# Kernel optimization log

Hardware: AMD Instinct MI355X
Metric: run time of the kernel (lower is better)

## Reference

```python
import jax, jax.numpy as jnp
import numpy as np

D_C = 16  # c // 4 with c = 64
BN_EPS = 1e-5


def _block(x, w, b, g, beta, m, v, a):
    """Conv2Dblock with 1x1 conv: pointwise conv -> BatchNorm2d (inference) -> PReLU."""
    y = jnp.einsum('oi,bift->boft', w, x) + b[None, :, None, None]
    scale = (g / jnp.sqrt(v + BN_EPS))[None, :, None, None]
    y = (y - m[None, :, None, None]) * scale + beta[None, :, None, None]
    return jnp.where(y >= 0, y, a * y)  # PReLU, single shared slope


def _asa(inp, fqkv, tqk, proj):
    b, c, f, t = inp.shape
    scale = 1.0 / np.sqrt(D_C)
    neg = -jnp.finfo(inp.dtype).max

    # frequency attention
    f_qkv = _block(inp, *fqkv)                      # [b, 3*d_c interleaved, f, t]
    f_qkv = f_qkv.reshape(b, D_C, 3, f, t)          # '(c k)' split, k fastest
    qf, kf, v = f_qkv[:, :, 0], f_qkv[:, :, 1], f_qkv[:, :, 2]
    f_score = jnp.einsum('bcft,bcyt->btfy', qf, kf) * scale
    f_score = jax.nn.softmax(f_score, axis=-1)
    f_out = jnp.einsum('btfy,bcyt->bcft', f_score, v)

    # causal time attention
    t_qk = _block(inp, *tqk)                        # [b, 2*d_c interleaved, f, t]
    t_qk = t_qk.reshape(b, D_C, 2, f, t)
    qt, kt = t_qk[:, :, 0], t_qk[:, :, 1]
    t_score = jnp.einsum('bcft,bcfy->bfty', qt, kt) * scale
    causal_mask = jnp.triu(jnp.ones((t, t), dtype=bool), 1)  # strictly upper => future
    t_score = jnp.where(causal_mask[None, None], neg, t_score)
    t_score = jax.nn.softmax(t_score, axis=-1)
    t_out = jnp.einsum('bfty,bcfy->bcft', t_score, f_out)

    out = _block(t_out, *proj)
    return out + inp


def setup_inputs() -> dict:
    key = jax.random.key(0)
    ks = jax.random.split(key, 24)
    B, C, F, T = 2, 64, 257, 500
    dc = D_C

    def conv_params(ki, kb, out_ch, in_ch):
        w = jax.random.normal(ki, (out_ch, in_ch), jnp.float32) * (1.0 / np.sqrt(in_ch))
        b = jax.random.normal(kb, (out_ch,), jnp.float32) * 0.02
        return w, b

    inp = jax.random.normal(ks[0], (B, C, F, T), jnp.float32)

    fqkv_w, fqkv_b = conv_params(ks[1], ks[2], 3 * dc, C)
    fqkv_g = 1.0 + 0.1 * jax.random.uniform(ks[3], (3 * dc,), jnp.float32)
    fqkv_beta = 0.02 * jax.random.normal(ks[4], (3 * dc,), jnp.float32)
    fqkv_m = 0.02 * jax.random.normal(ks[5], (3 * dc,), jnp.float32)
    fqkv_v = 0.9 + 0.2 * jax.random.uniform(ks[6], (3 * dc,), jnp.float32)
    fqkv_a = jnp.full((1,), 0.25, jnp.float32)

    tqk_w, tqk_b = conv_params(ks[7], ks[8], 2 * dc, C)
    tqk_g = 1.0 + 0.1 * jax.random.uniform(ks[9], (2 * dc,), jnp.float32)
    tqk_beta = 0.02 * jax.random.normal(ks[10], (2 * dc,), jnp.float32)
    tqk_m = 0.02 * jax.random.normal(ks[11], (2 * dc,), jnp.float32)
    tqk_v = 0.9 + 0.2 * jax.random.uniform(ks[12], (2 * dc,), jnp.float32)
    tqk_a = jnp.full((1,), 0.25, jnp.float32)

    proj_w, proj_b = conv_params(ks[13], ks[14], C, dc)
    proj_g = 1.0 + 0.1 * jax.random.uniform(ks[15], (C,), jnp.float32)
    proj_beta = 0.02 * jax.random.normal(ks[16], (C,), jnp.float32)
    proj_m = 0.02 * jax.random.normal(ks[17], (C,), jnp.float32)
    proj_v = 0.9 + 0.2 * jax.random.uniform(ks[18], (C,), jnp.float32)
    proj_a = jnp.full((1,), 0.25, jnp.float32)

    return dict(inp=inp,
                fqkv_w=fqkv_w, fqkv_b=fqkv_b, fqkv_g=fqkv_g, fqkv_beta=fqkv_beta,
                fqkv_m=fqkv_m, fqkv_v=fqkv_v, fqkv_a=fqkv_a,
                tqk_w=tqk_w, tqk_b=tqk_b, tqk_g=tqk_g, tqk_beta=tqk_beta,
                tqk_m=tqk_m, tqk_v=tqk_v, tqk_a=tqk_a,
                proj_w=proj_w, proj_b=proj_b, proj_g=proj_g, proj_beta=proj_beta,
                proj_m=proj_m, proj_v=proj_v, proj_a=proj_a)


def reference(inp, fqkv_w, fqkv_b, fqkv_g, fqkv_beta, fqkv_m, fqkv_v, fqkv_a,
              tqk_w, tqk_b, tqk_g, tqk_beta, tqk_m, tqk_v, tqk_a,
              proj_w, proj_b, proj_g, proj_beta, proj_m, proj_v, proj_a):
    return _asa(inp,
                (fqkv_w, fqkv_b, fqkv_g, fqkv_beta, fqkv_m, fqkv_v, fqkv_a),
                (tqk_w, tqk_b, tqk_g, tqk_beta, tqk_m, tqk_v, tqk_a),
                (proj_w, proj_b, proj_g, proj_beta, proj_m, proj_v, proj_a))
```

## Files before the change

### kernel.cpp

```cpp
#include <hip/hip_runtime.h>

#define BB 2
#define CIN 64
#define FD 257
#define TD 500
#define FT (FD*TD)
#define EPS 1e-5f
#define NEGINF (-3.0e38f)
#define FDP 260
#define FQT_PLANE (TD*FDP)
#define LOG2E 1.44269504088896f
#define EXP2F(x) __builtin_amdgcn_exp2f(x)

typedef _Float16 half_t;
typedef half_t half2_t __attribute__((ext_vector_type(2)));
typedef half_t half4 __attribute__((ext_vector_type(4)));
typedef float  f32x4 __attribute__((ext_vector_type(4)));

__global__ __launch_bounds__(256) void stage1_kernel(
    const float* __restrict__ x,
    const float* __restrict__ fw, const float* __restrict__ fb_,
    const float* __restrict__ fg, const float* __restrict__ fbe,
    const float* __restrict__ fm, const float* __restrict__ fv_,
    const float* __restrict__ fa,
    const float* __restrict__ tw, const float* __restrict__ tb_,
    const float* __restrict__ tg, const float* __restrict__ tbe,
    const float* __restrict__ tm, const float* __restrict__ tv_,
    const float* __restrict__ ta,
    half_t* __restrict__ fq, half_t* __restrict__ tq)
{
    __shared__ half_t Wh[80][68];
    __shared__ float  Bl[80];
    __shared__ half_t Ob[4][32][80];
    const int tid = threadIdx.x;
    for (int idx = tid; idx < 80*64; idx += 256) {
        const int o = idx >> 6, i = idx & 63;
        float sc, wv;
        if (o < 48) { sc = fg[o]*rsqrtf(fv_[o]+EPS); wv = fw[o*64+i]; }
        else { const int o2 = o-48; sc = tg[o2]*rsqrtf(tv_[o2]+EPS); wv = tw[o2*64+i]; }
        Wh[o][i] = (half_t)(wv*sc);
    }
    if (tid < 80) {
        const int o = tid;
        if (o < 48) Bl[o] = (fb_[o]-fm[o])*(fg[o]*rsqrtf(fv_[o]+EPS)) + fbe[o];
        else { const int o2 = o-48; Bl[o] = (tb_[o2]-tm[o2])*(tg[o2]*rsqrtf(tv_[o2]+EPS)) + tbe[o2]; }
    }
    __syncthreads();
    const float af = fa[0], at = ta[0];
    const int w = tid >> 6, lane = tid & 63;
    const int lmod = lane & 15, ldiv = lane >> 4;
    const int b  = blockIdx.x / 1004;
    const int nb = blockIdx.x % 1004;
    const long n0 = (long)nb*128;

    half4 a[5][4];
    #pragma unroll
    for (int ot = 0; ot < 5; ++ot)
        #pragma unroll
        for (int ks = 0; ks < 4; ++ks)
            a[ot][ks] = *(const half4*)&Wh[16*ot + lmod][16*ks + 4*ldiv];
    f32x4 bias[5];
    #pragma unroll
    for (int ot = 0; ot < 5; ++ot)
        #pragma unroll
        for (int r = 0; r < 4; ++r)
            bias[ot][r] = Bl[16*ot + 4*ldiv + r];

    const float* xplane = x + (long)b*CIN*FT;
    half4 bfr[2][4];
    #pragma unroll
    for (int pt = 0; pt < 2; ++pt) {
        const long p = n0 + 32*w + 16*pt + lmod;
        const long pc = (p < FT) ? p : (FT-1);
        const float* xp = xplane + pc;
        #pragma unroll
        for (int ks = 0; ks < 4; ++ks) {
            #pragma unroll
            for (int e = 0; e < 4; ++e) {
                const int ch = 16*ks + 4*ldiv + e;
                bfr[pt][ks][e] = (half_t)xp[(long)ch*FT];
            }
        }
    }
    #pragma unroll
    for (int pt = 0; pt < 2; ++pt) {
        const int pl = 16*pt + lmod;
        const int msk = ((pl >> 2) & 3) << 2;
        #pragma unroll
        for (int ot = 0; ot < 5; ++ot) {
            f32x4 acc = bias[ot];
            #pragma unroll
            for (int ks = 0; ks < 4; ++ks)
                acc = __builtin_amdgcn_mfma_f32_16x16x16f16(a[ot][ks], bfr[pt][ks], acc, 0, 0, 0);
            const float alpha = (ot < 3) ? af : at;
            half4 hv;
            #pragma unroll
            for (int r = 0; r < 4; ++r) {
                float v = acc[r];
                v = v >= 0.f ? v : alpha*v;
                hv[r] = (half_t)v;
            }
            *(half4*)&Ob[w][pl][(16*ot + 4*ldiv) ^ msk] = hv;
        }
    }
    const int pr = lane & 7, og0 = lane >> 3;
    const long pbase = n0 + 32*w + 4*pr;
    if (pbase < FT) {
        const int msk = (pr & 3) << 2;
        #pragma unroll
        for (int i = 0; i < 10; ++i) {
            const int o = og0 + 8*i;
            half4 hv;
            #pragma unroll
            for (int e = 0; e < 4; ++e) hv[e] = Ob[w][4*pr + e][o ^ msk];
            half_t* dst = (o < 48) ? (fq + ((long)b*48 + o)*FT + pbase)
                                   : (tq + ((long)b*32 + (o-48))*FT + pbase);
            *(half4*)dst = hv;
        }
    }
}

__global__ __launch_bounds__(256) void transpose_h2h_kernel(
    const half_t* __restrict__ src, half_t* __restrict__ dst,
    int R, int C, int CS, int RP)
{
    __shared__ half_t tile[64][68];
    const int plane = blockIdx.x;
    const int rb = blockIdx.y*64, cb = blockIdx.z*64;
    const half_t* s = src + (long)plane*R*CS;
    half_t* d = dst + (long)plane*C*RP;
    const int q4 = (threadIdx.x & 15)*4;
    const int wl = threadIdx.x >> 4;
    #pragma unroll
    for (int p = 0; p < 4; ++p) {
        const int r = rb + wl + 16*p;
        const int c = cb + q4;
        half4 v = {(half_t)0.f,(half_t)0.f,(half_t)0.f,(half_t)0.f};
        if (r < R) {
            const half_t* srow = s + (long)r*CS;
            if (c + 3 < C) v = *(const half4*)(srow + c);
            else {
                #pragma unroll
                for (int e = 0; e < 4; ++e) if (c+e < C) v[e] = srow[c+e];
            }
        }
        *(half4*)&tile[wl + 16*p][q4] = v;
    }
    __syncthreads();
    #pragma unroll
    for (int p = 0; p < 4; ++p) {
        const int c = cb + wl + 16*p;
        if (c >= C) continue;
        const int r0 = rb + q4;
        half4 o;
        #pragma unroll
        for (int e = 0; e < 4; ++e) o[e] = tile[q4 + e][wl + 16*p];
        half_t* drow = d + (long)c*RP;
        if (r0 + 3 < RP) *(half4*)(drow + r0) = o;
        else {
            #pragma unroll
            for (int e = 0; e < 4; ++e) if (r0+e < RP) drow[r0+e] = o[e];
        }
    }
}

__global__ __launch_bounds__(512) void fattn_kernel(
    const half_t* __restrict__ fqT, half_t* __restrict__ foT)
{
    __shared__ half_t KT[272*20];
    __shared__ half_t QT[272*20];
    __shared__ half_t Vs[16*280];
    const int tid = threadIdx.x;
    const int b = blockIdx.x / TD, t = blockIdx.x % TD;
    const half_t* base = fqT + (long)b*48*FQT_PLANE + (long)t*FDP;
    const half_t qsc = (half_t)(0.25f*LOG2E);
    for (int s = tid; s < 48*68; s += 512) {
        const int c3 = s / 68, j = s - c3*68;
        const int f0 = 4*j;
        half4 v = {(half_t)0.f,(half_t)0.f,(half_t)0.f,(half_t)0.f};
        if (f0 < FDP) v = *(const half4*)(base + (long)c3*FQT_PLANE + f0);
        const int c = c3 / 3, wh = c3 - 3*c;
        if (wh == 0) {
            #pragma unroll
            for (int e = 0; e < 4; ++e) QT[(f0+e)*20 + c] = v[e]*qsc;
        } else if (wh == 1) {
            #pragma unroll
            for (int e = 0; e < 4; ++e) KT[(f0+e)*20 + c] = v[e];
        } else {
            *(half4*)&Vs[c*280 + f0] = v;
        }
    }
    __syncthreads();
    const int w = tid >> 6, lane = tid & 63;
    const int lmod = lane & 15, ldiv = lane >> 4;
    for (int ft = w; ft < 17; ft += 8) {
        const int f0 = 16*ft;
        const half4 qb = *(const half4*)&QT[(f0+lmod)*20 + 4*ldiv];
        f32x4 o = {0.f,0.f,0.f,0.f};
        float m = NEGINF, l = 0.f;
        for (int yt = 0; yt < 16; yt += 2) {
            const int y0 = 16*yt;
            const half4 ka0 = *(const half4*)&KT[(y0   +lmod)*20 + 4*ldiv];
            const half4 ka1 = *(const half4*)&KT[(y0+16+lmod)*20 + 4*ldiv];
            f32x4 s0 = __builtin_amdgcn_mfma_f32_16x16x16f16(
                ka0, qb, (f32x4){0.f,0.f,0.f,0.f}, 0, 0, 0);
            f32x4 s1 = __builtin_amdgcn_mfma_f32_16x16x16f16(
                ka1, qb, (f32x4){0.f,0.f,0.f,0.f}, 0, 0, 0);
            float mt = fmaxf(fmaxf(fmaxf(s0[0],s0[1]), fmaxf(s0[2],s0[3])),
                             fmaxf(fmaxf(s1[0],s1[1]), fmaxf(s1[2],s1[3])));
            mt = fmaxf(mt, __shfl_xor(mt, 16, 64));
            mt = fmaxf(mt, __shfl_xor(mt, 32, 64));
            const float mn = fmaxf(m, mt);
            const float alpha = EXP2F(m - mn);
            half4 pb0, pb1; float ps = 0.f;
            #pragma unroll
            for (int r = 0; r < 4; ++r) {
                const float p0 = EXP2F(s0[r] - mn);
                const float p1 = EXP2F(s1[r] - mn);
                pb0[r] = (half_t)p0; pb1[r] = (half_t)p1;
                ps += p0 + p1;
            }
            ps += __shfl_xor(ps, 16, 64);
            ps += __shfl_xor(ps, 32, 64);
            l = l*alpha + ps;  m = mn;
            o[0] *= alpha; o[1] *= alpha; o[2] *= alpha; o[3] *= alpha;
            const half4 va0 = *(const half4*)&Vs[lmod*280 + y0      + 4*ldiv];
            const half4 va1 = *(const half4*)&Vs[lmod*280 + y0 + 16 + 4*ldiv];
            o = __builtin_amdgcn_mfma_f32_16x16x16f16(va0, pb0, o, 0, 0, 0);
            o = __builtin_amdgcn_mfma_f32_16x16x16f16(va1, pb1, o, 0, 0, 0);
        }
        {
            const int y0 = 256;
            const half4 ka = *(const half4*)&KT[(y0+lmod)*20 + 4*ldiv];
            f32x4 s = __builtin_amdgcn_mfma_f32_16x16x16f16(
                ka, qb, (f32x4){0.f,0.f,0.f,0.f}, 0, 0, 0);
            #pragma unroll
            for (int r = 0; r < 4; ++r)
                if (y0 + 4*ldiv + r >= FD) s[r] = NEGINF;
            float mt = fmaxf(fmaxf(s[0],s[1]), fmaxf(s[2],s[3]));
            mt = fmaxf(mt, __shfl_xor(mt, 16, 64));
            mt = fmaxf(mt, __shfl_xor(mt, 32, 64));
            const float mn = fmaxf(m, mt);
            const float alpha = EXP2F(m - mn);
            half4 pb; float ps = 0.f;
            #pragma unroll
            for (int r = 0; r < 4; ++r) {
                const float p = EXP2F(s[r] - mn);
                pb[r] = (half_t)p; ps += p;
            }
            ps += __shfl_xor(ps, 16, 64);
            ps += __shfl_xor(ps, 32, 64);
            l = l*alpha + ps;  m = mn;
            o[0] *= alpha; o[1] *= alpha; o[2] *= alpha; o[3] *= alpha;
            const half4 va = *(const half4*)&Vs[lmod*280 + y0 + 4*ldiv];
            o = __builtin_amdgcn_mfma_f32_16x16x16f16(va, pb, o, 0, 0, 0);
        }
        const float inv = 1.f/l;
        const int f = f0 + lmod;
        if (f < FD) {
            #pragma unroll
            for (int r = 0; r < 4; ++r) {
                const int c = 4*ldiv + r;
                foT[((long)(b*16 + c)*TD + t)*FDP + f] = (half_t)(o[r]*inv);
            }
        }
    }
}

__global__ __launch_bounds__(512) void tattn_kernel(
    const half_t* __restrict__ tq, const half_t* __restrict__ fo,
    float* __restrict__ tout)
{
    extern __shared__ half_t lds[];
    half_t* KT  = lds;
    half_t* FOs = KT + 512*20;
    const int tid = threadIdx.x;
    const int b = blockIdx.x / FD, f = blockIdx.x % FD;
    const int h = blockIdx.y;
    const half_t* qbase = tq + (long)b*32*FT + (long)f*TD;
    const half_t* fbase = fo + (long)b*16*FT + (long)f*TD;
    const half_t qsc = (half_t)(0.25f*LOG2E);
    const int shift = h ? 7 : 6;
    const int nq = 16 << shift;
    for (int idx = tid; idx < nq; idx += 512) {
        const int c = idx >> shift;
        const int y4 = (idx & ((1 << shift) - 1)) * 4;
        half4 kv = {(half_t)0.f,(half_t)0.f,(half_t)0.f,(half_t)0.f};
        half4 fv = kv;
        if (y4 + 3 < TD) {
            kv = *(const half4*)(qbase + (long)(2*c+1)*FT + y4);
            fv = *(const half4*)(fbase + (long)c*FT + y4);
        }
        #pragma unroll
        for (int e = 0; e < 4; ++e) KT[(y4+e)*20 + c] = kv[e];
        *(half4*)&FOs[c*520 + y4] = fv;
    }
    const int w = tid >> 6, lane = tid & 63;
    const int lmod = lane & 15, ldiv = lane >> 4;
    const int tts[2] = { h ? (16 + w) : w, h ? (31 - w) : (15 - w) };
    half4 qbr[2];
    #pragma unroll
    for (int i = 0; i < 2; ++i) {
        const int t = 16*tts[i] + lmod;
        #pragma unroll
        for (int e = 0; e < 4; ++e) {
            const int c = 4*ldiv + e;
            half_t qv = (half_t)0.f;
            if (t < TD) qv = qbase[(long)(2*c)*FT + t];
            qbr[i][e] = qv * qsc;
        }
    }
    __syncthreads();
    #pragma unroll
    for (int i = 0; i < 2; ++i) {
        const int tt = tts[i];
        const int t0 = 16*tt;
        const half4 qb = qbr[i];
        f32x4 o = {0.f,0.f,0.f,0.f};
        float m = NEGINF, l = 0.f;
        int yt = 0;
        for (; yt + 1 < tt; yt += 2) {
            const int y0 = 16*yt;
            const half4 ka0 = *(const half4*)&KT[(y0   +lmod)*20 + 4*ldiv];
            const half4 ka1 = *(const half4*)&KT[(y0+16+lmod)*20 + 4*ldiv];
            f32x4 s0 = __builtin_amdgcn_mfma_f32_16x16x16f16(
                ka0, qb, (f32x4){0.f,0.f,0.f,0.f}, 0, 0, 0);
            f32x4 s1 = __builtin_amdgcn_mfma_f32_16x16x16f16(
                ka1, qb, (f32x4){0.f,0.f,0.f,0.f}, 0, 0, 0);
            float mt = fmaxf(fmaxf(fmaxf(s0[0],s0[1]), fmaxf(s0[2],s0[3])),
                             fmaxf(fmaxf(s1[0],s1[1]), fmaxf(s1[2],s1[3])));
            mt = fmaxf(mt, __shfl_xor(mt, 16, 64));
            mt = fmaxf(mt, __shfl_xor(mt, 32, 64));
            const float mn = fmaxf(m, mt);
            const float alpha = EXP2F(m - mn);
            half4 pb0, pb1; float ps = 0.f;
            #pragma unroll
            for (int r = 0; r < 4; ++r) {
                const float p0 = EXP2F(s0[r] - mn);
                const float p1 = EXP2F(s1[r] - mn);
                pb0[r] = (half_t)p0; pb1[r] = (half_t)p1;
                ps += p0 + p1;
            }
            ps += __shfl_xor(ps, 16, 64);
            ps += __shfl_xor(ps, 32, 64);
            l = l*alpha + ps;  m = mn;
            o[0] *= alpha; o[1] *= alpha; o[2] *= alpha; o[3] *= alpha;
            const half4 fa0 = *(const half4*)&FOs[lmod*520 + y0      + 4*ldiv];
            const half4 fa1 = *(const half4*)&FOs[lmod*520 + y0 + 16 + 4*ldiv];
            o = __builtin_amdgcn_mfma_f32_16x16x16f16(fa0, pb0, o, 0, 0, 0);
            o = __builtin_amdgcn_mfma_f32_16x16x16f16(fa1, pb1, o, 0, 0, 0);
        }
        if (yt < tt) {
            const int y0 = 16*yt;
            const half4 ka0 = *(const half4*)&KT[(y0   +lmod)*20 + 4*ldiv];
            const half4 ka1 = *(const half4*)&KT[(y0+16+lmod)*20 + 4*ldiv];
            f32x4 s0 = __builtin_amdgcn_mfma_f32_16x16x16f16(
                ka0, qb, (f32x4){0.f,0.f,0.f,0.f}, 0, 0, 0);
            f32x4 s1 = __builtin_amdgcn_mfma_f32_16x16x16f16(
                ka1, qb, (f32x4){0.f,0.f,0.f,0.f}, 0, 0, 0);
            #pragma unroll
            for (int r = 0; r < 4; ++r)
                if (4*ldiv + r > lmod) s1[r] = NEGINF;
            float mt = fmaxf(fmaxf(fmaxf(s0[0],s0[1]), fmaxf(s0[2],s0[3])),
                             fmaxf(fmaxf(s1[0],s1[1]), fmaxf(s1[2],s1[3])));
            mt = fmaxf(mt, __shfl_xor(mt, 16, 64));
            mt = fmaxf(mt, __shfl_xor(mt, 32, 64));
            const float mn = fmaxf(m, mt);
            const float alpha = EXP2F(m - mn);
            half4 pb0, pb1; float ps = 0.f;
            #pragma unroll
            for (int r = 0; r < 4; ++r) {
                const float p0 = EXP2F(s0[r] - mn);
                const float p1 = EXP2F(s1[r] - mn);
                pb0[r] = (half_t)p0; pb1[r] = (half_t)p1;
                ps += p0 + p1;
            }
            ps += __shfl_xor(ps, 16, 64);
            ps += __shfl_xor(ps, 32, 64);
            l = l*alpha + ps;  m = mn;
            o[0] *= alpha; o[1] *= alpha; o[2] *= alpha; o[3] *= alpha;
            const half4 fa0 = *(const half4*)&FOs[lmod*520 + y0      + 4*ldiv];
            const half4 fa1 = *(const half4*)&FOs[lmod*520 + y0 + 16 + 4*ldiv];
            o = __builtin_amdgcn_mfma_f32_16x16x16f16(fa0, pb0, o, 0, 0, 0);
            o = __builtin_amdgcn_mfma_f32_16x16x16f16(fa1, pb1, o, 0, 0, 0);
        } else {
            const int y0 = 16*tt;
            const half4 ka = *(const half4*)&KT[(y0+lmod)*20 + 4*ldiv];
            f32x4 s = __builtin_amdgcn_mfma_f32_16x16x16f16(
                ka, qb, (f32x4){0.f,0.f,0.f,0.f}, 0, 0, 0);
            #pragma unroll
            for (int r = 0; r < 4; ++r)
                if (4*ldiv + r > lmod) s[r] = NEGINF;
            float mt = fmaxf(fmaxf(s[0],s[1]), fmaxf(s[2],s[3]));
            mt = fmaxf(mt, __shfl_xor(mt, 16, 64));
            mt = fmaxf(mt, __shfl_xor(mt, 32, 64));
            const float mn = fmaxf(m, mt);
            const float alpha = EXP2F(m - mn);
            half4 pb; float ps = 0.f;
            #pragma unroll
            for (int r = 0; r < 4; ++r) {
                const float p = EXP2F(s[r] - mn);
                pb[r] = (half_t)p; ps += p;
            }
            ps += __shfl_xor(ps, 16, 64);
            ps += __shfl_xor(ps, 32, 64);
            l = l*alpha + ps;  m = mn;
            o[0] *= alpha; o[1] *= alpha; o[2] *= alpha; o[3] *= alpha;
            const half4 fa4 = *(const half4*)&FOs[lmod*520 + y0 + 4*ldiv];
            o = __builtin_amdgcn_mfma_f32_16x16x16f16(fa4, pb, o, 0, 0, 0);
        }
        const float inv = 1.f/l;
        const int t = t0 + lmod;
        if (t < TD) {
            #pragma unroll
            for (int r = 0; r < 4; ++r) {
                const int c = 4*ldiv + r;
                tout[((long)(b*16 + c)*FD + f)*TD + t] = o[r]*inv;
            }
        }
    }
}

__global__ __launch_bounds__(256) void proj_kernel(
    const float* __restrict__ tout, const float* __restrict__ x,
    const float* __restrict__ pw, const float* __restrict__ pb_,
    const float* __restrict__ pg, const float* __restrict__ pbe,
    const float* __restrict__ pm, const float* __restrict__ pv_,
    const float* __restrict__ pa,
    float* __restrict__ out)
{
    __shared__ float PW[32*16];
    __shared__ float PB[32];
    const int tid = threadIdx.x;
    const int cg   = blockIdx.x & 1;
    const int bidx = blockIdx.x >> 1;
    const int ob   = cg*32;
    for (int idx = tid; idx < 32*16; idx += 256) {
        const int ol = idx >> 4;
        const int o = ob + ol;
        PW[idx] = pw[o*16 + (idx & 15)]*(pg[o]*rsqrtf(pv_[o]+EPS));
    }
    if (tid < 32) {
        const int o = ob + tid;
        PB[tid] = (pb_[o]-pm[o])*(pg[o]*rsqrtf(pv_[o]+EPS)) + pbe[o];
    }
    __syncthreads();
    const float ap = pa[0];
    const int og = tid >> 6, lane = tid & 63;
    const int b  = bidx / 502;
    const int nb = bidx % 502;
    const long n0 = (long)nb*256 + lane*4;
    if (n0 >= FT) return;
    float4 acc[8];
    #pragma unroll
    for (int j = 0; j < 8; ++j) {
        const float bv = PB[og*8+j];
        acc[j] = make_float4(bv, bv, bv, bv);
    }
    const float* tb = tout + (long)b*16*FT + n0;
    for (int cc = 0; cc < 16; cc += 4) {
        const float* tc = tb + (long)cc*FT;
        const float4 t0 = *(const float4*)(tc);
        const float4 t1 = *(const float4*)(tc + FT);
        const float4 t2 = *(const float4*)(tc + 2*FT);
        const float4 t3 = *(const float4*)(tc + 3*FT);
        #pragma unroll
        for (int j = 0; j < 8; ++j) {
            const float4 wv = *(const float4*)&PW[(og*8+j)*16 + cc];
            acc[j].x += wv.x*t0.x + wv.y*t1.x + wv.z*t2.x + wv.w*t3.x;
            acc[j].y += wv.x*t0.y + wv.y*t1.y + wv.z*t2.y + wv.w*t3.y;
            acc[j].z += wv.x*t0.z + wv.y*t1.z + wv.z*t2.z + wv.w*t3.z;
            acc[j].w += wv.x*t0.w + wv.y*t1.w + wv.z*t2.w + wv.w*t3.w;
        }
    }
    #pragma unroll
    for (int j = 0; j < 8; ++j) {
        const int o = ob + og*8 + j;
        float4 v = acc[j];
        v.x = v.x >= 0.f ? v.x : ap*v.x;
        v.y = v.y >= 0.f ? v.y : ap*v.y;
        v.z = v.z >= 0.f ? v.z : ap*v.z;
        v.w = v.w >= 0.f ? v.w : ap*v.w;
        const long gi = (long)(b*64 + o)*FT + n0;
        const float4 xv = *(const float4*)(x + gi);
        v.x += xv.x; v.y += xv.y; v.z += xv.z; v.w += xv.w;
        *(float4*)(out + gi) = v;
    }
}

extern "C" void kernel_launch(void* const* d_in, const int* in_sizes, int n_in,
                              void* d_out, int out_size, void* d_ws, size_t ws_size,
                              hipStream_t stream)
{
    const float* x     = (const float*)d_in[0];
    const float* fw    = (const float*)d_in[1];
    const float* fb_   = (const float*)d_in[2];
    const float* fg    = (const float*)d_in[3];
    const float* fbe   = (const float*)d_in[4];
    const float* fm    = (const float*)d_in[5];
    const float* fv_   = (const float*)d_in[6];
    const float* fa    = (const float*)d_in[7];
    const float* tw    = (const float*)d_in[8];
    const float* tb_   = (const float*)d_in[9];
    const float* tg    = (const float*)d_in[10];
    const float* tbe   = (const float*)d_in[11];
    const float* tm    = (const float*)d_in[12];
    const float* tv_   = (const float*)d_in[13];
    const float* ta    = (const float*)d_in[14];
    const float* pw    = (const float*)d_in[15];
    const float* pb_   = (const float*)d_in[16];
    const float* pg    = (const float*)d_in[17];
    const float* pbe   = (const float*)d_in[18];
    const float* pm    = (const float*)d_in[19];
    const float* pv_   = (const float*)d_in[20];
    const float* pa    = (const float*)d_in[21];
    float* out = (float*)d_out;

    char* base = (char*)d_ws;
    const size_t szA = (size_t)BB*48*FT*sizeof(half_t);
    const size_t szB = (size_t)BB*16*FT*sizeof(half_t);
    const size_t szC = (size_t)BB*32*FT*sizeof(half_t);
    const size_t szD = (size_t)96*FQT_PLANE*sizeof(half_t);
    const size_t need = szA + szB + szC + szD;
    if (ws_size < need) return;
    half_t* fqh  = (half_t*)base;
    half_t* foTh = (half_t*)base;
    half_t* foh  = (half_t*)(base + szA);
    half_t* tqh  = (half_t*)(base + szA + szB);
    half_t* fqTh = (half_t*)(base + szA + szB + szC);
    float*  tout = (float*)(base + szA + szB + szC);

    stage1_kernel<<<dim3(BB*1004), dim3(256), 0, stream>>>(
        x, fw, fb_, fg, fbe, fm, fv_, fa, tw, tb_, tg, tbe, tm, tv_, ta, fqh, tqh);

    transpose_h2h_kernel<<<dim3(BB*48, 5, 8), dim3(256), 0, stream>>>(
        fqh, fqTh, FD, TD, TD, FDP);

    fattn_kernel<<<dim3(BB*TD), dim3(512), 0, stream>>>(fqTh, foTh);

    transpose_h2h_kernel<<<dim3(BB*16, 8, 5), dim3(256), 0, stream>>>(
        foTh, foh, TD, FD, FDP, TD);

    const int tlds = (512*20 + 16*520)*(int)sizeof(half_t);
    (void)hipFuncSetAttribute(reinterpret_cast<const void*>(tattn_kernel),
                        hipFuncAttributeMaxDynamicSharedMemorySize, tlds);
    tattn_kernel<<<dim3(BB*FD, 2), dim3(512), tlds, stream>>>(tqh, foh, tout);

    proj_kernel<<<dim3(BB*502*2), dim3(256), 0, stream>>>(
        tout, x, pw, pb_, pg, pbe, pm, pv_, pa, out);
}
```

Baseline: 281.2 us.

## Fuse output projection, BN, PReLU and residual into time-attention kernel

Result: faster. 263.6 us (-6.2%).

```diff
diff --git a/kernel.cpp b/kernel.cpp
--- a/kernel.cpp
+++ b/kernel.cpp
@@ -269,17 +269,31 @@
 
 __global__ __launch_bounds__(512) void tattn_kernel(
     const half_t* __restrict__ tq, const half_t* __restrict__ fo,
-    float* __restrict__ tout)
+    const float* __restrict__ pw, const float* __restrict__ pb_,
+    const float* __restrict__ pg, const float* __restrict__ pbe,
+    const float* __restrict__ pm, const float* __restrict__ pv_,
+    const float* __restrict__ pal,
+    const float* __restrict__ x, float* __restrict__ out)
 {
     extern __shared__ half_t lds[];
     half_t* KT  = lds;
     half_t* FOs = KT + 512*20;
+    half_t* PWh = FOs + 16*520;
+    float*  PBl = (float*)(PWh + 64*20);
     const int tid = threadIdx.x;
     const int b = blockIdx.x / FD, f = blockIdx.x % FD;
     const int h = blockIdx.y;
     const half_t* qbase = tq + (long)b*32*FT + (long)f*TD;
     const half_t* fbase = fo + (long)b*16*FT + (long)f*TD;
     const half_t qsc = (half_t)(0.25f*LOG2E);
+    if (tid < 64) {
+        const int o64 = tid;
+        const float sc = pg[o64]*rsqrtf(pv_[o64]+EPS);
+        PBl[o64] = (pb_[o64]-pm[o64])*sc + pbe[o64];
+        #pragma unroll
+        for (int c = 0; c < 16; ++c)
+            PWh[o64*20 + c] = (half_t)(pw[o64*16 + c]*sc);
+    }
     const int shift = h ? 7 : 6;
     const int nq = 16 << shift;
     for (int idx = tid; idx < nq; idx += 512) {
@@ -310,6 +324,7 @@
             qbr[i][e] = qv * qsc;
         }
     }
+    const float app = pal[0];
     __syncthreads();
     #pragma unroll
     for (int i = 0; i < 2; ++i) {
@@ -411,80 +426,30 @@
         }
         const float inv = 1.f/l;
         const int t = t0 + lmod;
-        if (t < TD) {
-            #pragma unroll
-            for (int r = 0; r < 4; ++r) {
-                const int c = 4*ldiv + r;
-                tout[((long)(b*16 + c)*FD + f)*TD + t] = o[r]*inv;
-            }
-        }
-    }
-}
-
-__global__ __launch_bounds__(256) void proj_kernel(
-    const float* __restrict__ tout, const float* __restrict__ x,
-    const float* __restrict__ pw, const float* __restrict__ pb_,
-    const float* __restrict__ pg, const float* __restrict__ pbe,
-    const float* __restrict__ pm, const float* __restrict__ pv_,
-    const float* __restrict__ pa,
-    float* __restrict__ out)
-{
-    __shared__ float PW[32*16];
-    __shared__ float PB[32];
-    const int tid = threadIdx.x;
-    const int cg   = blockIdx.x & 1;
-    const int bidx = blockIdx.x >> 1;
-    const int ob   = cg*32;
-    for (int idx = tid; idx < 32*16; idx += 256) {
-        const int ol = idx >> 4;
-        const int o = ob + ol;
-        PW[idx] = pw[o*16 + (idx & 15)]*(pg[o]*rsqrtf(pv_[o]+EPS));
-    }
-    if (tid < 32) {
-        const int o = ob + tid;
-        PB[tid] = (pb_[o]-pm[o])*(pg[o]*rsqrtf(pv_[o]+EPS)) + pbe[o];
-    }
-    __syncthreads();
-    const float ap = pa[0];
-    const int og = tid >> 6, lane = tid & 63;
-    const int b  = bidx / 502;
-    const int nb = bidx % 502;
-    const long n0 = (long)nb*256 + lane*4;
-    if (n0 >= FT) return;
-    float4 acc[8];
-    #pragma unroll
-    for (int j = 0; j < 8; ++j) {
-        const float bv = PB[og*8+j];
-        acc[j] = make_float4(bv, bv, bv, bv);
-    }
-    const float* tb = tout + (long)b*16*FT + n0;
-    for (int cc = 0; cc < 16; cc += 4) {
-        const float* tc = tb + (long)cc*FT;
-        const float4 t0 = *(const float4*)(tc);
-        const float4 t1 = *(const float4*)(tc + FT);
-        const float4 t2 = *(const float4*)(tc + 2*FT);
-        const float4 t3 = *(const float4*)(tc + 3*FT);
-        #pragma unroll
-        for (int j = 0; j < 8; ++j) {
-            const float4 wv = *(const float4*)&PW[(og*8+j)*16 + cc];
-            acc[j].x += wv.x*t0.x + wv.y*t1.x + wv.z*t2.x + wv.w*t3.x;
-            acc[j].y += wv.x*t0.y + wv.y*t1.y + wv.z*t2.y + wv.w*t3.y;
-            acc[j].z += wv.x*t0.z + wv.y*t1.z + wv.z*t2.z + wv.w*t3.z;
-            acc[j].w += wv.x*t0.w + wv.y*t1.w + wv.z*t2.w + wv.w*t3.w;
-        }
-    }
-    #pragma unroll
-    for (int j = 0; j < 8; ++j) {
-        const int o = ob + og*8 + j;
-        float4 v = acc[j];
-        v.x = v.x >= 0.f ? v.x : ap*v.x;
-        v.y = v.y >= 0.f ? v.y : ap*v.y;
-        v.z = v.z >= 0.f ? v.z : ap*v.z;
-        v.w = v.w >= 0.f ? v.w : ap*v.w;
-        const long gi = (long)(b*64 + o)*FT + n0;
-        const float4 xv = *(const float4*)(x + gi);
-        v.x += xv.x; v.y += xv.y; v.z += xv.z; v.w += xv.w;
-        *(float4*)(out + gi) = v;
+        const bool tok = (t < TD);
+        half4 tb;
+        #pragma unroll
+        for (int r = 0; r < 4; ++r)
+            tb[r] = tok ? (half_t)(o[r]*inv) : (half_t)0.f;
+        const long gbase = (long)(b*64)*FT + (long)f*TD + t;
+        #pragma unroll
+        for (int ot = 0; ot < 4; ++ot) {
+            const half4 pf = *(const half4*)&PWh[(16*ot + lmod)*20 + 4*ldiv];
+            f32x4 a2;
+            #pragma unroll
+            for (int r = 0; r < 4; ++r) a2[r] = PBl[16*ot + 4*ldiv + r];
+            a2 = __builtin_amdgcn_mfma_f32_16x16x16f16(pf, tb, a2, 0, 0, 0);
+            if (tok) {
+                #pragma unroll
+                for (int r = 0; r < 4; ++r) {
+                    const int o64 = 16*ot + 4*ldiv + r;
+                    float v = a2[r];
+                    v = v >= 0.f ? v : app*v;
+                    const long gi = gbase + (long)o64*FT;
+                    out[gi] = v + x[gi];
+                }
+            }
+        }
     }
 }
 
@@ -528,7 +493,6 @@
     half_t* foh  = (half_t*)(base + szA);
     half_t* tqh  = (half_t*)(base + szA + szB);
     half_t* fqTh = (half_t*)(base + szA + szB + szC);
-    float*  tout = (float*)(base + szA + szB + szC);
 
     stage1_kernel<<<dim3(BB*1004), dim3(256), 0, stream>>>(
         x, fw, fb_, fg, fbe, fm, fv_, fa, tw, tb_, tg, tbe, tm, tv_, ta, fqh, tqh);
@@ -541,11 +505,10 @@
     transpose_h2h_kernel<<<dim3(BB*16, 8, 5), dim3(256), 0, stream>>>(
         foTh, foh, TD, FD, FDP, TD);
 
-    const int tlds = (512*20 + 16*520)*(int)sizeof(half_t);
+    const int tlds = (512*20 + 16*520 + 64*20)*(int)sizeof(half_t)
+                   + 64*(int)sizeof(float);
     (void)hipFuncSetAttribute(reinterpret_cast<const void*>(tattn_kernel),
                         hipFuncAttributeMaxDynamicSharedMemorySize, tlds);
-    tattn_kernel<<<dim3(BB*FD, 2), dim3(512), tlds, stream>>>(tqh, foh, tout);
-
-    proj_kernel<<<dim3(BB*502*2), dim3(256), 0, stream>>>(
-        tout, x, pw, pb_, pg, pbe, pm, pv_, pa, out);
+    tattn_kernel<<<dim3(BB*FD, 2), dim3(512), tlds, stream>>>(
+        tqh, foh, pw, pb_, pg, pbe, pm, pv_, pa, x, out);
 }
```
